# Performance work log

Hardware: AMD Instinct MI355X
Metric: run time of the kernel (lower is better)

## Reference

```python
import jax, jax.numpy as jnp
import numpy as np

GOP = 4

def _resize_bilinear(x, Ho, Wo):
    # x: (M, C, Hs, Ws); matches F.interpolate(mode='bilinear', align_corners=False)
    M, C, Hs, Ws = x.shape
    ys = jnp.clip((jnp.arange(Ho, dtype=jnp.float32) + 0.5) * (Hs / Ho) - 0.5, 0.0, Hs - 1.0)
    xs = jnp.clip((jnp.arange(Wo, dtype=jnp.float32) + 0.5) * (Ws / Wo) - 0.5, 0.0, Ws - 1.0)
    y0 = jnp.floor(ys).astype(jnp.int32); y1 = jnp.minimum(y0 + 1, Hs - 1)
    x0 = jnp.floor(xs).astype(jnp.int32); x1 = jnp.minimum(x0 + 1, Ws - 1)
    wy = (ys - y0)[None, None, :, None]
    wx = (xs - x0)[None, None, None, :]
    r0 = x[:, :, y0, :]; r1 = x[:, :, y1, :]
    top = r0[:, :, :, x0] * (1 - wx) + r0[:, :, :, x1] * wx
    bot = r1[:, :, :, x0] * (1 - wx) + r1[:, :, :, x1] * wx
    return top * (1 - wy) + bot * wy

def _deform_sample(feat, flow):
    # feat: (M,C,H,W); flow: (M,2,H,W), ch0=dy, ch1=dx (torchvision deform_conv order).
    # Bilinear sample at (y+dy, x+dx) with zero padding outside (kernel_size=1 deform conv).
    M, C, H, W = feat.shape
    gy = jnp.arange(H, dtype=flow.dtype)[:, None]
    gx = jnp.arange(W, dtype=flow.dtype)[None, :]
    y = gy + flow[:, 0]; x = gx + flow[:, 1]          # (M,H,W)
    y0f = jnp.floor(y); x0f = jnp.floor(x)
    wy = (y - y0f)[:, None]; wx = (x - x0f)[:, None]  # (M,1,H,W)
    y0 = y0f.astype(jnp.int32); x0 = x0f.astype(jnp.int32)
    feat_flat = feat.reshape(M, C, H * W)
    def gather(yi, xi):
        valid = ((yi >= 0) & (yi < H) & (xi >= 0) & (xi < W)).astype(feat.dtype)
        idx = (jnp.clip(yi, 0, H - 1) * W + jnp.clip(xi, 0, W - 1)).reshape(M, H * W)
        v = jnp.take_along_axis(feat_flat, jnp.broadcast_to(idx[:, None, :], (M, C, H * W)), axis=2)
        return v.reshape(M, C, H, W) * valid[:, None]
    v00 = gather(y0, x0);     v01 = gather(y0, x0 + 1)
    v10 = gather(y0 + 1, x0); v11 = gather(y0 + 1, x0 + 1)
    return v00 * (1 - wy) * (1 - wx) + v01 * (1 - wy) * wx + v10 * wy * (1 - wx) + v11 * wy * wx

def setup_inputs():
    key = jax.random.key(0)
    k = jax.random.split(key, 7)
    B, T, Himg, Wimg = 4, 16, 256, 256
    num_gop = T // GOP      # 4
    t = GOP - 1             # 3 P-frames per GOP
    C_in, D, h, w = 256, 256, 64, 64
    imgs = jnp.zeros((B, T, 3, Himg, Wimg), jnp.float32)
    i_features = jax.random.normal(k[0], (B * num_gop, C_in, h, w), jnp.float32)
    # flows of a few pixels at image scale (scaled by 0.25 inside forward)
    p_motions = jax.random.normal(k[1], (B, num_gop * t, 2, Himg, Wimg), jnp.float32) * 8.0
    W_emb = jax.random.normal(k[2], (D, C_in), jnp.float32) * 0.02
    b_emb = jax.random.normal(k[3], (D,), jnp.float32) * 0.02
    W_dc = jax.random.normal(k[4], (D, D), jnp.float32) * 0.02
    b_dc = jax.random.normal(k[5], (D,), jnp.float32) * 0.02
    return {"imgs": imgs, "i_features": i_features, "p_motions": p_motions,
            "W_emb": W_emb, "b_emb": b_emb, "W_dc": W_dc, "b_dc": b_dc}

def reference(imgs, i_features, p_motions, W_emb, b_emb, W_dc, b_dc):
    B = imgs.shape[0]
    num_gop = imgs.shape[1] // GOP
    # 1x1 embedding conv
    feat = jnp.einsum('mchw,oc->mohw', i_features, W_emb) + b_emb[None, :, None, None]
    M0, D, h, w = feat.shape
    scale = w / imgs.shape[-1]
    Tp = p_motions.shape[1]
    flow = _resize_bilinear(p_motions.reshape(B * Tp, 2, p_motions.shape[-2], p_motions.shape[-1]), h, w) * scale
    t = Tp // num_gop
    # repeat each GOP's I-frame features for its t P-frame flows
    feat = jnp.broadcast_to(feat.reshape(B, num_gop, 1, D, h, w), (B, num_gop, t, D, h, w)).reshape(-1, D, h, w)
    flow = flow.reshape(-1, 2, h, w)
    # flow-guided deformable conv with 1x1 kernel: bilinear gather + 1x1 projection
    samp = _deform_sample(feat, flow)
    out = jnp.einsum('mchw,oc->mohw', samp, W_dc) + b_dc[None, :, None, None]
    # adaptive_avg_pool2d(.,1).flatten(3)
    return out.mean(axis=(-2, -1)).reshape(B, num_gop, t, D)
```

## Files before the change

### kernel.cpp

```cpp
#include <hip/hip_runtime.h>
#include <math.h>

#define HW 4096
#define CIN 256
#define DD 256
#define M_TOTAL 48
#define NSP 4
#define SPPX (HW / NSP)

__global__ __launch_bounds__(256) void k_pre(
    const float* __restrict__ p_motions,
    const float* __restrict__ W_emb,
    const float* __restrict__ b_emb,
    const float* __restrict__ W_dc,
    float* __restrict__ Ag,
    float* __restrict__ Sg,
    float* __restrict__ WT,
    float* __restrict__ bfold)
{
    const int tid = threadIdx.x;
    const int bid = blockIdx.x;

    if (bid < M_TOTAL * NSP) {
        __shared__ float Al[HW];
        __shared__ float red[4];
        const int m = bid >> 2;
        const int sp = bid & 3;
        const float4* p0 = (const float4*)(p_motions + (size_t)m * 2 * 65536);
        const float4* p1 = p0 + 65536 / 4;

        for (int i = tid; i < HW; i += 256) Al[i] = 0.f;
        __syncthreads();

        #pragma unroll
        for (int ii = 0; ii < SPPX / 256; ++ii) {
            const int i = ii * 256 + tid;
            const int y = sp * 16 + (i >> 6);
            const int x = i & 63;
            const int r1 = 4 * y + 1, r2 = 4 * y + 2;
            const float4 v10 = p0[r1 * 64 + x];
            const float4 v20 = p0[r2 * 64 + x];
            const float4 v11 = p1[r1 * 64 + x];
            const float4 v21 = p1[r2 * 64 + x];
            const float fy = (v10.y + v10.z + v20.y + v20.z) * 0.0625f;
            const float fx = (v11.y + v11.z + v21.y + v21.z) * 0.0625f;

            const float yy = (float)y + fy;
            const float xx = (float)x + fx;
            const float y0f = floorf(yy), x0f = floorf(xx);
            const float wy = yy - y0f, wx = xx - x0f;
            const int iy0 = (int)y0f, ix0 = (int)x0f;
            const int iy1 = iy0 + 1, ix1 = ix0 + 1;
            const float w00 = (1.f - wy) * (1.f - wx);
            const float w01 = (1.f - wy) * wx;
            const float w10 = wy * (1.f - wx);
            const float w11 = wy * wx;
            const bool y0ok = (iy0 >= 0) & (iy0 < 64);
            const bool y1ok = (iy1 >= 0) & (iy1 < 64);
            const bool x0ok = (ix0 >= 0) & (ix0 < 64);
            const bool x1ok = (ix1 >= 0) & (ix1 < 64);
            if (y0ok & x0ok) atomicAdd(&Al[iy0 * 64 + ix0], w00);
            if (y0ok & x1ok) atomicAdd(&Al[iy0 * 64 + ix1], w01);
            if (y1ok & x0ok) atomicAdd(&Al[iy1 * 64 + ix0], w10);
            if (y1ok & x1ok) atomicAdd(&Al[iy1 * 64 + ix1], w11);
        }
        __syncthreads();

        float part = 0.f;
        float* AgM = Ag + (size_t)m * HW;
        for (int i = tid; i < HW; i += 256) {
            const float v = Al[i];
            part += v;
            if (v != 0.f) atomicAdd(&AgM[i], v);
        }
        for (int off = 32; off > 0; off >>= 1) part += __shfl_down(part, off, 64);
        if ((tid & 63) == 0) red[tid >> 6] = part;
        __syncthreads();
        if (tid == 0) atomicAdd(&Sg[m], red[0] + red[1] + red[2] + red[3]);
    } else {
        __shared__ float wdc[256];
        __shared__ float red2[4];
        const int o = bid - M_TOTAL * NSP;
        wdc[tid] = W_dc[(size_t)o * 256 + tid];
        __syncthreads();
        float acc = 0.f;
        #pragma unroll 8
        for (int k = 0; k < 256; ++k)
            acc += wdc[k] * W_emb[(size_t)k * 256 + tid];
        WT[(size_t)tid * 256 + o] = acc;

        float pb = wdc[tid] * b_emb[tid];
        for (int off = 32; off > 0; off >>= 1) pb += __shfl_down(pb, off, 64);
        if ((tid & 63) == 0) red2[tid >> 6] = pb;
        __syncthreads();
        if (tid == 0) bfold[o] = red2[0] + red2[1] + red2[2] + red2[3];
    }
}

__global__ __launch_bounds__(256, 4) void k_gather_dot(
    const float* __restrict__ i_features,
    const float* __restrict__ Ag,
    float* __restrict__ gpart)
{
    const int fm = blockIdx.x;
    const int chunk = blockIdx.y;
    const int sp = blockIdx.z;
    const int tid = threadIdx.x;
    const int wave = tid >> 6, lane = tid & 63;
    const int m0 = fm * 3;

    const float4* A0 = (const float4*)(Ag + (size_t)(m0 + 0) * HW + sp * SPPX);
    const float4* A1 = (const float4*)(Ag + (size_t)(m0 + 1) * HW + sp * SPPX);
    const float4* A2 = (const float4*)(Ag + (size_t)(m0 + 2) * HW + sp * SPPX);
    float4 a0[4], a1[4], a2[4];
    #pragma unroll
    for (int k = 0; k < 4; ++k) {
        a0[k] = A0[lane + 64 * k];
        a1[k] = A1[lane + 64 * k];
        a2[k] = A2[lane + 64 * k];
    }

    #pragma unroll
    for (int c = 0; c < 4; ++c) {
        const int ci = chunk * 16 + wave * 4 + c;
        const float4* f4 = (const float4*)(i_features + ((size_t)fm * CIN + ci) * HW + sp * SPPX);
        float s0 = 0.f, s1 = 0.f, s2 = 0.f;
        #pragma unroll
        for (int k = 0; k < 4; ++k) {
            const float4 v = f4[lane + 64 * k];
            s0 += v.x * a0[k].x + v.y * a0[k].y + v.z * a0[k].z + v.w * a0[k].w;
            s1 += v.x * a1[k].x + v.y * a1[k].y + v.z * a1[k].z + v.w * a1[k].w;
            s2 += v.x * a2[k].x + v.y * a2[k].y + v.z * a2[k].z + v.w * a2[k].w;
        }
        #pragma unroll
        for (int off = 32; off > 0; off >>= 1) {
            s0 += __shfl_down(s0, off, 64);
            s1 += __shfl_down(s1, off, 64);
            s2 += __shfl_down(s2, off, 64);
        }
        if (lane == 0) {
            gpart[((size_t)sp * M_TOTAL + m0 + 0) * CIN + ci] = s0;
            gpart[((size_t)sp * M_TOTAL + m0 + 1) * CIN + ci] = s1;
            gpart[((size_t)sp * M_TOTAL + m0 + 2) * CIN + ci] = s2;
        }
    }
}

__global__ __launch_bounds__(256) void k_out(
    const float* __restrict__ gpart,
    const float* __restrict__ Sg,
    const float* __restrict__ WT,
    const float* __restrict__ bfold,
    const float* __restrict__ b_dc,
    float* __restrict__ out)
{
    __shared__ float gl[CIN];
    const int m = blockIdx.x;
    const int tid = threadIdx.x;

    float gv = 0.f;
    for (int sp = 0; sp < NSP; ++sp)
        gv += gpart[((size_t)sp * M_TOTAL + m) * CIN + tid];
    gl[tid] = gv * (1.f / 4096.f);
    __syncthreads();

    const float Sm = Sg[m] * (1.f / 4096.f);
    float acc = 0.f;
    #pragma unroll 8
    for (int ci = 0; ci < CIN; ++ci)
        acc += gl[ci] * WT[(size_t)ci * DD + tid];
    out[(size_t)m * DD + tid] = acc + bfold[tid] * Sm + b_dc[tid];
}

extern "C" void kernel_launch(void* const* d_in, const int* in_sizes, int n_in,
                              void* d_out, int out_size, void* d_ws, size_t ws_size,
                              hipStream_t stream) {
    const float* i_features = (const float*)d_in[1];
    const float* p_motions  = (const float*)d_in[2];
    const float* W_emb      = (const float*)d_in[3];
    const float* b_emb      = (const float*)d_in[4];
    const float* W_dc       = (const float*)d_in[5];
    const float* b_dc       = (const float*)d_in[6];
    float* out = (float*)d_out;

    float* ws = (float*)d_ws;
    float* Ag    = ws;
    float* Sg    = Ag + (size_t)M_TOTAL * HW;
    float* WT    = Sg + 64;
    float* bfold = WT + 65536;
    float* gpart = bfold + 256;

    hipMemsetAsync(Ag, 0, ((size_t)M_TOTAL * HW + 64) * sizeof(float), stream);

    k_pre<<<M_TOTAL * NSP + DD, 256, 0, stream>>>(p_motions, W_emb, b_emb, W_dc,
                                                  Ag, Sg, WT, bfold);
    dim3 g2(16, 16, NSP);
    k_gather_dot<<<g2, 256, 0, stream>>>(i_features, Ag, gpart);
    k_out<<<M_TOTAL, 256, 0, stream>>>(gpart, Sg, WT, bfold, b_dc, out);
}
```

Measured before the change: 170.3 us.

## Replace atomics with per-slice partials and fuse output projection into gather kernel

k_pre now writes each spatial slice's scatter-weight map and sum to its own buffer with plain float4 stores, instead of atomically accumulating into a shared map. This removes the memset and the global atomics. The gather kernel sums the four partial maps on load. It then applies its slice of the folded projection directly, accumulating into the output with atomics, so the separate k_out launch goes away. In exchange it reads four times more map data per block, adds many output atomics, and depends on k_pre zeroing the output first.

```diff
diff --git a/kernel.cpp b/kernel.cpp
--- a/kernel.cpp
+++ b/kernel.cpp
@@ -13,10 +13,11 @@
     const float* __restrict__ W_emb,
     const float* __restrict__ b_emb,
     const float* __restrict__ W_dc,
-    float* __restrict__ Ag,
-    float* __restrict__ Sg,
+    float* __restrict__ Ag4,
+    float* __restrict__ Sg4,
     float* __restrict__ WT,
-    float* __restrict__ bfold)
+    float* __restrict__ bfold,
+    float* __restrict__ out)
 {
     const int tid = threadIdx.x;
     const int bid = blockIdx.x;
@@ -66,22 +67,25 @@
         }
         __syncthreads();
 
+        const float4* Al4 = (const float4*)Al;
+        float4* dst = (float4*)(Ag4 + (size_t)(m * NSP + sp) * HW);
         float part = 0.f;
-        float* AgM = Ag + (size_t)m * HW;
-        for (int i = tid; i < HW; i += 256) {
-            const float v = Al[i];
-            part += v;
-            if (v != 0.f) atomicAdd(&AgM[i], v);
+        #pragma unroll
+        for (int i = tid; i < HW / 4; i += 256) {
+            const float4 v = Al4[i];
+            dst[i] = v;
+            part += v.x + v.y + v.z + v.w;
         }
         for (int off = 32; off > 0; off >>= 1) part += __shfl_down(part, off, 64);
         if ((tid & 63) == 0) red[tid >> 6] = part;
         __syncthreads();
-        if (tid == 0) atomicAdd(&Sg[m], red[0] + red[1] + red[2] + red[3]);
+        if (tid == 0) Sg4[m * NSP + sp] = red[0] + red[1] + red[2] + red[3];
     } else {
         __shared__ float wdc[256];
         __shared__ float red2[4];
         const int o = bid - M_TOTAL * NSP;
         wdc[tid] = W_dc[(size_t)o * 256 + tid];
+        if (tid < 48) out[(size_t)o * 48 + tid] = 0.f;
         __syncthreads();
         float acc = 0.f;
         #pragma unroll 8
@@ -97,11 +101,16 @@
     }
 }
 
-__global__ __launch_bounds__(256, 4) void k_gather_dot(
+__global__ __launch_bounds__(256, 4) void k_gather_out(
     const float* __restrict__ i_features,
-    const float* __restrict__ Ag,
-    float* __restrict__ gpart)
+    const float* __restrict__ Ag4,
+    const float* __restrict__ Sg4,
+    const float* __restrict__ WT,
+    const float* __restrict__ bfold,
+    const float* __restrict__ b_dc,
+    float* __restrict__ out)
 {
+    __shared__ float gl[3][16];
     const int fm = blockIdx.x;
     const int chunk = blockIdx.y;
     const int sp = blockIdx.z;
@@ -109,15 +118,24 @@
     const int wave = tid >> 6, lane = tid & 63;
     const int m0 = fm * 3;
 
-    const float4* A0 = (const float4*)(Ag + (size_t)(m0 + 0) * HW + sp * SPPX);
-    const float4* A1 = (const float4*)(Ag + (size_t)(m0 + 1) * HW + sp * SPPX);
-    const float4* A2 = (const float4*)(Ag + (size_t)(m0 + 2) * HW + sp * SPPX);
-    float4 a0[4], a1[4], a2[4];
+    float4 a[3][4];
     #pragma unroll
-    for (int k = 0; k < 4; ++k) {
-        a0[k] = A0[lane + 64 * k];
-        a1[k] = A1[lane + 64 * k];
-        a2[k] = A2[lane + 64 * k];
+    for (int j = 0; j < 3; ++j) {
+        const float4* P0 = (const float4*)(Ag4 + ((size_t)((m0 + j) * NSP + 0)) * HW + sp * SPPX);
+        const float4* P1 = (const float4*)(Ag4 + ((size_t)((m0 + j) * NSP + 1)) * HW + sp * SPPX);
+        const float4* P2 = (const float4*)(Ag4 + ((size_t)((m0 + j) * NSP + 2)) * HW + sp * SPPX);
+        const float4* P3 = (const float4*)(Ag4 + ((size_t)((m0 + j) * NSP + 3)) * HW + sp * SPPX);
+        #pragma unroll
+        for (int k = 0; k < 4; ++k) {
+            const float4 t0 = P0[lane + 64 * k];
+            const float4 t1 = P1[lane + 64 * k];
+            const float4 t2 = P2[lane + 64 * k];
+            const float4 t3 = P3[lane + 64 * k];
+            a[j][k].x = t0.x + t1.x + t2.x + t3.x;
+            a[j][k].y = t0.y + t1.y + t2.y + t3.y;
+            a[j][k].z = t0.z + t1.z + t2.z + t3.z;
+            a[j][k].w = t0.w + t1.w + t2.w + t3.w;
+        }
     }
 
     #pragma unroll
@@ -128,9 +146,9 @@
         #pragma unroll
         for (int k = 0; k < 4; ++k) {
             const float4 v = f4[lane + 64 * k];
-            s0 += v.x * a0[k].x + v.y * a0[k].y + v.z * a0[k].z + v.w * a0[k].w;
-            s1 += v.x * a1[k].x + v.y * a1[k].y + v.z * a1[k].z + v.w * a1[k].w;
-            s2 += v.x * a2[k].x + v.y * a2[k].y + v.z * a2[k].z + v.w * a2[k].w;
+            s0 += v.x * a[0][k].x + v.y * a[0][k].y + v.z * a[0][k].z + v.w * a[0][k].w;
+            s1 += v.x * a[1][k].x + v.y * a[1][k].y + v.z * a[1][k].z + v.w * a[1][k].w;
+            s2 += v.x * a[2][k].x + v.y * a[2][k].y + v.z * a[2][k].z + v.w * a[2][k].w;
         }
         #pragma unroll
         for (int off = 32; off > 0; off >>= 1) {
@@ -139,37 +157,36 @@
             s2 += __shfl_down(s2, off, 64);
         }
         if (lane == 0) {
-            gpart[((size_t)sp * M_TOTAL + m0 + 0) * CIN + ci] = s0;
-            gpart[((size_t)sp * M_TOTAL + m0 + 1) * CIN + ci] = s1;
-            gpart[((size_t)sp * M_TOTAL + m0 + 2) * CIN + ci] = s2;
-        }
-    }
-}
-
-__global__ __launch_bounds__(256) void k_out(
-    const float* __restrict__ gpart,
-    const float* __restrict__ Sg,
-    const float* __restrict__ WT,
-    const float* __restrict__ bfold,
-    const float* __restrict__ b_dc,
-    float* __restrict__ out)
-{
-    __shared__ float gl[CIN];
-    const int m = blockIdx.x;
-    const int tid = threadIdx.x;
-
-    float gv = 0.f;
-    for (int sp = 0; sp < NSP; ++sp)
-        gv += gpart[((size_t)sp * M_TOTAL + m) * CIN + tid];
-    gl[tid] = gv * (1.f / 4096.f);
+            gl[0][wave * 4 + c] = s0;
+            gl[1][wave * 4 + c] = s1;
+            gl[2][wave * 4 + c] = s2;
+        }
+    }
     __syncthreads();
 
-    const float Sm = Sg[m] * (1.f / 4096.f);
-    float acc = 0.f;
-    #pragma unroll 8
-    for (int ci = 0; ci < CIN; ++ci)
-        acc += gl[ci] * WT[(size_t)ci * DD + tid];
-    out[(size_t)m * DD + tid] = acc + bfold[tid] * Sm + b_dc[tid];
+    const int o = tid;
+    float acc0 = 0.f, acc1 = 0.f, acc2 = 0.f;
+    #pragma unroll
+    for (int q = 0; q < 16; ++q) {
+        const float wv = WT[(size_t)(chunk * 16 + q) * DD + o];
+        acc0 += gl[0][q] * wv;
+        acc1 += gl[1][q] * wv;
+        acc2 += gl[2][q] * wv;
+    }
+    const float inv = 1.f / 4096.f;
+    atomicAdd(&out[(size_t)(m0 + 0) * DD + o], acc0 * inv);
+    atomicAdd(&out[(size_t)(m0 + 1) * DD + o], acc1 * inv);
+    atomicAdd(&out[(size_t)(m0 + 2) * DD + o], acc2 * inv);
+
+    if (chunk == 0 && sp == 0) {
+        #pragma unroll
+        for (int j = 0; j < 3; ++j) {
+            const int m = m0 + j;
+            const float Sm = (Sg4[m * NSP + 0] + Sg4[m * NSP + 1] +
+                              Sg4[m * NSP + 2] + Sg4[m * NSP + 3]) * inv;
+            atomicAdd(&out[(size_t)m * DD + tid], bfold[tid] * Sm + b_dc[tid]);
+        }
+    }
 }
 
 extern "C" void kernel_launch(void* const* d_in, const int* in_sizes, int n_in,
@@ -184,17 +201,13 @@
     float* out = (float*)d_out;
 
     float* ws = (float*)d_ws;
-    float* Ag    = ws;
-    float* Sg    = Ag + (size_t)M_TOTAL * HW;
-    float* WT    = Sg + 64;
+    float* Ag4   = ws;
+    float* Sg4   = Ag4 + (size_t)M_TOTAL * NSP * HW;
+    float* WT    = Sg4 + 256;
     float* bfold = WT + 65536;
-    float* gpart = bfold + 256;
-
-    hipMemsetAsync(Ag, 0, ((size_t)M_TOTAL * HW + 64) * sizeof(float), stream);
 
     k_pre<<<M_TOTAL * NSP + DD, 256, 0, stream>>>(p_motions, W_emb, b_emb, W_dc,
-                                                  Ag, Sg, WT, bfold);
+                                                  Ag4, Sg4, WT, bfold, out);
     dim3 g2(16, 16, NSP);
-    k_gather_dot<<<g2, 256, 0, stream>>>(i_features, Ag, gpart);
-    k_out<<<M_TOTAL, 256, 0, stream>>>(gpart, Sg, WT, bfold, b_dc, out);
+    k_gather_out<<<g2, 256, 0, stream>>>(i_features, Ag4, Sg4, WT, bfold, b_dc, out);
 }
```

After: 157.4 us (median of 2 runs). 7.6% less time.
